# Kernel optimization log

Measured on AMD Instinct MI355X. Metric: run time of the kernel, lower is better.

The kernel has to match this reference:

```python
import jax, jax.numpy as jnp
import numpy as np

S, B, I, H = 2048, 64, 256, 128  # seq, batch, sent_size, hidden


def setup_inputs() -> dict:
    key = jax.random.key(0)
    ks = jax.random.split(key, 12)
    s = 1.0 / np.sqrt(H)
    u = lambda k, shape: jax.random.uniform(k, shape, jnp.float32, -s, s)
    return {
        "inp": jax.random.normal(ks[0], (S, B, I), jnp.float32),
        "hid_state": jax.random.normal(ks[1], (2, B, H), jnp.float32),
        "w_ih_f": u(ks[2], (3 * H, I)), "w_hh_f": u(ks[3], (3 * H, H)),
        "b_ih_f": u(ks[4], (3 * H,)), "b_hh_f": u(ks[5], (3 * H,)),
        "w_ih_b": u(ks[6], (3 * H, I)), "w_hh_b": u(ks[7], (3 * H, H)),
        "b_ih_b": u(ks[8], (3 * H,)), "b_hh_b": u(ks[9], (3 * H,)),
        "attn_w": u(ks[10], (2 * H, 2 * H)), "attn_b": jnp.zeros((2 * H,), jnp.float32),
        "comb_w": u(ks[11], (2 * H, 2 * H)),
    }


def _gru_dir(x, h0, w_ih, w_hh, b_ih, b_hh):
    # x: (S,B,I); precompute input-side gates once: (S,B,3H)
    xg = jnp.einsum('sbi,gi->sbg', x, w_ih) + b_ih

    def step(h, xg_t):
        gh = h @ w_hh.T + b_hh
        xr, xz, xn = jnp.split(xg_t, 3, axis=-1)
        hr, hz, hn = jnp.split(gh, 3, axis=-1)
        r = jax.nn.sigmoid(xr + hr)
        z = jax.nn.sigmoid(xz + hz)
        n = jnp.tanh(xn + r * hn)
        h_new = (1.0 - z) * n + z * h
        return h_new, h_new

    hT, outs = jax.lax.scan(step, h0, xg)
    return outs, hT


def reference(inp, hid_state, w_ih_f, w_hh_f, b_ih_f, b_hh_f,
              w_ih_b, w_hh_b, b_ih_b, b_hh_b, attn_w, attn_b, comb_w):
    out_f, hT_f = _gru_dir(inp, hid_state[0], w_ih_f, w_hh_f, b_ih_f, b_hh_f)
    out_b_rev, hT_b = _gru_dir(inp[::-1], hid_state[1], w_ih_b, w_hh_b, b_ih_b, b_hh_b)
    out_state = jnp.concatenate([out_f, out_b_rev[::-1]], axis=-1)  # (S,B,2H)
    hid_out = jnp.stack([hT_f, hT_b], axis=0)  # (2,B,H)
    sent_annotation = out_state @ attn_w.T + attn_b
    # NB: original applies softmax over dim=1 (the batch axis) — kept faithfully.
    attn = jax.nn.softmax(sent_annotation @ comb_w.T, axis=1)
    # fused multiply-reduce over seq (replaces the O(n) cat loop)
    sent = jnp.sum(attn * out_state, axis=0, keepdims=True)  # (1,B,2H)
    return sent, hid_out
```

## Files before the change

kernel.cpp:

```cpp
#include <hip/hip_runtime.h>
#include <cstdint>
#include <cstddef>

#define S_LEN 2048
#define BATCH 64
#define ISZ   256
#define HSZ   128

typedef __attribute__((ext_vector_type(8))) short short8;
typedef __attribute__((ext_vector_type(4))) float f32x4;

__device__ __forceinline__ uint32_t bfh(float x)
{
    uint32_t u = __float_as_uint(x);
    u += 0x7fffu + ((u >> 16) & 1u);
    return u >> 16;
}
__device__ __forceinline__ unsigned short f2bf(float x) { return (unsigned short)bfh(x); }

__device__ __forceinline__ void stage_tile(const float* __restrict__ src, int row0,
                                           int K, int k0, int tid,
                                           short* __restrict__ hi, short* __restrict__ lo)
{
    #pragma unroll
    for (int it = 0; it < 4; ++it) {
        const int g   = tid + it * 256;
        const int row = g >> 3;
        const int kg  = (g & 7) * 8;
        const float* p = src + (size_t)(row0 + row) * K + k0 + kg;
        const float4 v0 = *reinterpret_cast<const float4*>(p);
        const float4 v1 = *reinterpret_cast<const float4*>(p + 4);
        const float f[8] = {v0.x, v0.y, v0.z, v0.w, v1.x, v1.y, v1.z, v1.w};
        uint32_t hp[4], lp[4];
        #pragma unroll
        for (int i = 0; i < 4; ++i) {
            const uint32_t h0 = bfh(f[2*i]), h1 = bfh(f[2*i+1]);
            const float r0 = f[2*i]   - __uint_as_float(h0 << 16);
            const float r1 = f[2*i+1] - __uint_as_float(h1 << 16);
            hp[i] = h0 | (h1 << 16);
            lp[i] = bfh(r0) | (bfh(r1) << 16);
        }
        *reinterpret_cast<uint4*>(&hi[row*72 + kg]) = make_uint4(hp[0], hp[1], hp[2], hp[3]);
        *reinterpret_cast<uint4*>(&lo[row*72 + kg]) = make_uint4(lp[0], lp[1], lp[2], lp[3]);
    }
}

template<int LAYOUT>
__global__ __launch_bounds__(256, 2)
void gemm_mfma(const float* __restrict__ A, const float* __restrict__ W,
               const float* __restrict__ bias, float* __restrict__ C,
               int M, int N, int K)
{
    __shared__ short As_hi[128*72];
    __shared__ short As_lo[128*72];
    __shared__ short Ws_hi[128*72];
    __shared__ short Ws_lo[128*72];

    const int tid = threadIdx.x;
    const int wv  = tid >> 6;
    const int l   = tid & 63;
    const int fr  = l & 15;
    const int fk  = (l >> 4) * 8;
    const int m0  = blockIdx.y * 128;
    const int n0  = blockIdx.x * 128;

    f32x4 acc[2][8] = {};

    for (int k0 = 0; k0 < K; k0 += 64) {
        stage_tile(A, m0, K, k0, tid, As_hi, As_lo);
        stage_tile(W, n0, K, k0, tid, Ws_hi, Ws_lo);
        __syncthreads();

        #pragma unroll
        for (int ks = 0; ks < 64; ks += 32) {
            short8 ah[2], al[2], bh[8], bl[8];
            #pragma unroll
            for (int mt = 0; mt < 2; ++mt) {
                const int r = (wv*32 + mt*16 + fr) * 72 + ks + fk;
                ah[mt] = *reinterpret_cast<const short8*>(&As_hi[r]);
                al[mt] = *reinterpret_cast<const short8*>(&As_lo[r]);
            }
            #pragma unroll
            for (int nt = 0; nt < 8; ++nt) {
                const int r = (nt*16 + fr) * 72 + ks + fk;
                bh[nt] = *reinterpret_cast<const short8*>(&Ws_hi[r]);
                bl[nt] = *reinterpret_cast<const short8*>(&Ws_lo[r]);
            }
            #pragma unroll
            for (int mt = 0; mt < 2; ++mt) {
                #pragma unroll
                for (int nt = 0; nt < 8; ++nt) {
                    acc[mt][nt] = __builtin_amdgcn_mfma_f32_16x16x32_bf16(
                        ah[mt], bh[nt], acc[mt][nt], 0, 0, 0);
                    acc[mt][nt] = __builtin_amdgcn_mfma_f32_16x16x32_bf16(
                        ah[mt], bl[nt], acc[mt][nt], 0, 0, 0);
                    acc[mt][nt] = __builtin_amdgcn_mfma_f32_16x16x32_bf16(
                        al[mt], bh[nt], acc[mt][nt], 0, 0, 0);
                }
            }
        }
        __syncthreads();
    }

    const int orow = (l >> 4) * 4;
    #pragma unroll
    for (int nt = 0; nt < 8; ++nt) {
        const int n = n0 + nt*16 + fr;
        const float bv = bias ? bias[n] : 0.f;
        #pragma unroll
        for (int mt = 0; mt < 2; ++mt) {
            const int mbase = m0 + wv*32 + mt*16 + orow;
            const f32x4 a = acc[mt][nt];
            if (LAYOUT == 0) {
                #pragma unroll
                for (int r = 0; r < 4; ++r)
                    C[(size_t)(mbase + r) * N + n] = a[r] + bv;
            } else {
                float4 o;
                o.x = a[0] + bv; o.y = a[1] + bv; o.z = a[2] + bv; o.w = a[3] + bv;
                *reinterpret_cast<float4*>(
                    &C[(size_t)(mbase >> 6) * ((size_t)N * 64) +
                       (size_t)n * 64 + (mbase & 63)]) = o;
            }
        }
    }
}

#define GRU_NB 4

__global__ __launch_bounds__(512, 2)
void gru_mfma(const float* __restrict__ xg_f, const float* __restrict__ xg_b,
              const float* __restrict__ whh_f, const float* __restrict__ whh_b,
              const float* __restrict__ bhh_f, const float* __restrict__ bhh_b,
              const float* __restrict__ h0,
              float* __restrict__ outs,
              float* __restrict__ hid_out)
{
    const int tid = threadIdx.x;
    const int wv  = tid >> 6;
    const int l   = tid & 63;
    const int dir = blockIdx.x >> 4;
    const int bb  = blockIdx.x & 15;
    const int b0  = bb * GRU_NB;

    const float* xg  = dir ? xg_b  : xg_f;
    const float* whh = dir ? whh_b : whh_f;
    const float* bhh = dir ? bhh_b : bhh_f;

    __shared__ short hhi[16 * 136];
    __shared__ short hlo[16 * 136];
    __shared__ float gate[16 * 388];

    short8 afr[3][4];
    {
        const int arow = wv * 48 + (l & 15);
        const int akof = (l >> 4) * 8;
        #pragma unroll
        for (int rt = 0; rt < 3; ++rt) {
            #pragma unroll
            for (int ks = 0; ks < 4; ++ks) {
                const float* p = whh + (size_t)(arow + rt*16) * 128 + ks*32 + akof;
                const float4 v0 = *reinterpret_cast<const float4*>(p);
                const float4 v1 = *reinterpret_cast<const float4*>(p + 4);
                short8 s;
                s[0] = f2bf(v0.x); s[1] = f2bf(v0.y); s[2] = f2bf(v0.z); s[3] = f2bf(v0.w);
                s[4] = f2bf(v1.x); s[5] = f2bf(v1.y); s[6] = f2bf(v1.z); s[7] = f2bf(v1.w);
                afr[rt][ks] = s;
            }
        }
    }

    const int aj = tid & 127;
    const int ab = tid >> 7;
    const float bh_r = bhh[aj];
    const float bh_z = bhh[128 + aj];
    const float bh_n = bhh[256 + aj];

    for (int i = tid; i < 16 * 136; i += 512) { hhi[i] = 0; hlo[i] = 0; }
    __syncthreads();

    float hj = h0[dir * (64*128) + (b0 + ab) * 128 + aj];
    {
        const uint32_t hb = bfh(hj);
        hhi[ab * 136 + aj] = (short)hb;
        hlo[ab * 136 + aj] = (short)f2bf(hj - __uint_as_float(hb << 16));
    }
    float xr, xz, xn;
    {
        const int s0 = dir ? (S_LEN - 1) : 0;
        const float* xrow = xg + ((size_t)s0 * 64 + b0 + ab) * 384;
        xr = xrow[aj]; xz = xrow[aj + 128]; xn = xrow[aj + 256];
    }
    __syncthreads();

    const int brow = (l & 15) * 136;
    const int bkof = (l >> 4) * 8;
    const int gcol = (l & 15) * 388;
    const int grow0 = wv * 48 + (l >> 4) * 4;

    for (int t = 0; t < S_LEN; ++t) {
        float pxr = 0.f, pxz = 0.f, pxn = 0.f;
        if (t + 1 < S_LEN) {
            const int s1 = dir ? (S_LEN - 2 - t) : (t + 1);
            const float* xrow = xg + ((size_t)s1 * 64 + b0 + ab) * 384;
            pxr = xrow[aj]; pxz = xrow[aj + 128]; pxn = xrow[aj + 256];
        }

        f32x4 acc[3] = {};
        #pragma unroll
        for (int ks = 0; ks < 4; ++ks) {
            const short8 bh8 = *reinterpret_cast<const short8*>(&hhi[brow + ks*32 + bkof]);
            const short8 bl8 = *reinterpret_cast<const short8*>(&hlo[brow + ks*32 + bkof]);
            #pragma unroll
            for (int rt = 0; rt < 3; ++rt) {
                acc[rt] = __builtin_amdgcn_mfma_f32_16x16x32_bf16(afr[rt][ks], bh8, acc[rt], 0, 0, 0);
                acc[rt] = __builtin_amdgcn_mfma_f32_16x16x32_bf16(afr[rt][ks], bl8, acc[rt], 0, 0, 0);
            }
        }
        #pragma unroll
        for (int rt = 0; rt < 3; ++rt) {
            float4 o;
            o.x = acc[rt][0]; o.y = acc[rt][1]; o.z = acc[rt][2]; o.w = acc[rt][3];
            *reinterpret_cast<float4*>(&gate[gcol + grow0 + rt*16]) = o;
        }

        asm volatile("s_waitcnt lgkmcnt(0)" ::: "memory");
        __builtin_amdgcn_s_barrier();

        const float hr = gate[ab*388 + aj]       + bh_r;
        const float hz = gate[ab*388 + 128 + aj] + bh_z;
        const float hn = gate[ab*388 + 256 + aj] + bh_n;
        const float r = 1.f / (1.f + __expf(-(xr + hr)));
        const float z = 1.f / (1.f + __expf(-(xz + hz)));
        const float x2 = xn + r * hn;
        const float ax = fabsf(x2);
        const float e  = __expf(-2.f * ax);
        const float nn = copysignf((1.f - e) / (1.f + e), x2);
        const float hnew = nn + z * (hj - nn);
        hj = hnew;

        const int s = dir ? (S_LEN - 1 - t) : t;
        outs[((size_t)s * 64 + b0 + ab) * 256 + dir * 128 + aj] = hnew;

        const uint32_t hb = bfh(hnew);
        hhi[ab * 136 + aj] = (short)hb;
        hlo[ab * 136 + aj] = (short)f2bf(hnew - __uint_as_float(hb << 16));
        xr = pxr; xz = pxz; xn = pxn;

        asm volatile("s_waitcnt lgkmcnt(0)" ::: "memory");
        __builtin_amdgcn_s_barrier();
    }

    hid_out[dir * (64*128) + (b0 + ab) * 128 + aj] = hj;
}

__global__ __launch_bounds__(256)
void attn_reduce(const float* __restrict__ lt,
                 const float* __restrict__ outs,
                 float* __restrict__ part)
{
    __shared__ float ltile[64 * 64];
    __shared__ float otile[64 * 65];

    const int tid  = threadIdx.x;
    const int lane = tid & 63;
    const int wv   = tid >> 6;
    const int c0   = blockIdx.x * 64;
    const int sc   = blockIdx.y;

    float acc[16];
    #pragma unroll
    for (int i = 0; i < 16; ++i) acc[i] = 0.f;

    for (int si = 0; si < 32; ++si) {
        const int s = sc * 32 + si;

        const float4* src = reinterpret_cast<const float4*>(
            lt + (size_t)s * 16384 + (size_t)c0 * 64);
        #pragma unroll
        for (int i = 0; i < 4; ++i)
            reinterpret_cast<float4*>(ltile)[tid + i * 256] = src[tid + i * 256];

        #pragma unroll
        for (int i = 0; i < 4; ++i) {
            int idx = tid + i * 256;
            int bb = idx >> 4, c4 = (idx & 15) * 4;
            float4 v = *reinterpret_cast<const float4*>(
                &outs[((size_t)s * 64 + bb) * 256 + c0 + c4]);
            otile[bb*65 + c4+0] = v.x; otile[bb*65 + c4+1] = v.y;
            otile[bb*65 + c4+2] = v.z; otile[bb*65 + c4+3] = v.w;
        }
        __syncthreads();

        #pragma unroll
        for (int ci = 0; ci < 16; ++ci) {
            int c = wv * 16 + ci;
            float x = ltile[c * 64 + lane];
            float m = x;
            #pragma unroll
            for (int off = 32; off; off >>= 1)
                m = fmaxf(m, __shfl_xor(m, off));
            float e = __expf(x - m);
            float ssum = e;
            #pragma unroll
            for (int off = 32; off; off >>= 1)
                ssum += __shfl_xor(ssum, off);
            float attn = e / ssum;
            acc[ci] += attn * otile[lane * 65 + c];
        }
        __syncthreads();
    }

    #pragma unroll
    for (int ci = 0; ci < 16; ++ci) {
        int c = wv * 16 + ci;
        part[(size_t)sc * 16384 + (size_t)lane * 256 + c0 + c] = acc[ci];
    }
}

__global__ __launch_bounds__(256)
void reduce_part(const float* __restrict__ part, float* __restrict__ sent)
{
    int idx = blockIdx.x * 256 + threadIdx.x;
    float s = 0.f;
    for (int sc = 0; sc < 64; ++sc)
        s += part[(size_t)sc * 16384 + idx];
    sent[idx] = s;
}

extern "C" void kernel_launch(void* const* d_in, const int* in_sizes, int n_in,
                              void* d_out, int out_size, void* d_ws, size_t ws_size,
                              hipStream_t stream)
{
    const float* inp    = (const float*)d_in[0];
    const float* hid0   = (const float*)d_in[1];
    const float* w_ih_f = (const float*)d_in[2];
    const float* w_hh_f = (const float*)d_in[3];
    const float* b_ih_f = (const float*)d_in[4];
    const float* b_hh_f = (const float*)d_in[5];
    const float* w_ih_b = (const float*)d_in[6];
    const float* w_hh_b = (const float*)d_in[7];
    const float* b_ih_b = (const float*)d_in[8];
    const float* b_hh_b = (const float*)d_in[9];
    const float* attn_w = (const float*)d_in[10];
    const float* attn_b = (const float*)d_in[11];
    const float* comb_w = (const float*)d_in[12];

    float* out = (float*)d_out;

    char* ws = (char*)d_ws;
    const size_t XG_BYTES = (size_t)S_LEN * BATCH * 384 * 4;
    const size_t OS_BYTES = (size_t)S_LEN * BATCH * 256 * 4;
    if (ws_size < 2 * XG_BYTES + OS_BYTES) return;

    float* xg_f   = (float*)(ws);
    float* xg_b   = (float*)(ws + XG_BYTES);
    float* outs   = (float*)(ws + 2 * XG_BYTES);
    float* sa     = (float*)(ws);
    float* logits = (float*)(ws + XG_BYTES);
    float* part   = (float*)(ws);

    const int M = S_LEN * BATCH;
    dim3 blk(256);

    gemm_mfma<0><<<dim3(3, 1024), blk, 0, stream>>>(inp, w_ih_f, b_ih_f, xg_f, M, 384, 256);
    gemm_mfma<0><<<dim3(3, 1024), blk, 0, stream>>>(inp, w_ih_b, b_ih_b, xg_b, M, 384, 256);

    gru_mfma<<<dim3(32), dim3(512), 0, stream>>>(
        xg_f, xg_b, w_hh_f, w_hh_b, b_hh_f, b_hh_b, hid0, outs, out + 16384);

    gemm_mfma<0><<<dim3(2, 1024), blk, 0, stream>>>(outs, attn_w, attn_b, sa, M, 256, 256);

    gemm_mfma<1><<<dim3(2, 1024), blk, 0, stream>>>(sa, comb_w, nullptr, logits, M, 256, 256);

    attn_reduce<<<dim3(4, 64), blk, 0, stream>>>(logits, outs, part);

    reduce_part<<<dim3(64), blk, 0, stream>>>(part, out);
}
```

Baseline: 2.796 ms.

## Remap GRU gate rows per wave and double-buffer hidden state to drop a barrier

```diff
diff --git a/kernel.cpp b/kernel.cpp
--- a/kernel.cpp
+++ b/kernel.cpp
@@ -127,6 +127,22 @@
 }
 
 #define GRU_NB 4
+#define HPAD   144
+
+__device__ __forceinline__ void store_h4(short* __restrict__ hi, short* __restrict__ lo,
+                                         int off, float4 h)
+{
+    const uint32_t b0 = bfh(h.x), b1 = bfh(h.y), b2 = bfh(h.z), b3 = bfh(h.w);
+    ushort4 hv, lv;
+    hv.x = (unsigned short)b0; hv.y = (unsigned short)b1;
+    hv.z = (unsigned short)b2; hv.w = (unsigned short)b3;
+    lv.x = f2bf(h.x - __uint_as_float(b0 << 16));
+    lv.y = f2bf(h.y - __uint_as_float(b1 << 16));
+    lv.z = f2bf(h.z - __uint_as_float(b2 << 16));
+    lv.w = f2bf(h.w - __uint_as_float(b3 << 16));
+    *reinterpret_cast<ushort4*>(&hi[off]) = hv;
+    *reinterpret_cast<ushort4*>(&lo[off]) = lv;
+}
 
 __global__ __launch_bounds__(512, 2)
 void gru_mfma(const float* __restrict__ xg_f, const float* __restrict__ xg_b,
@@ -140,118 +156,126 @@
     const int wv  = tid >> 6;
     const int l   = tid & 63;
     const int dir = blockIdx.x >> 4;
-    const int bb  = blockIdx.x & 15;
-    const int b0  = bb * GRU_NB;
+    const int b0  = (blockIdx.x & 15) * GRU_NB;
 
     const float* xg  = dir ? xg_b  : xg_f;
     const float* whh = dir ? whh_b : whh_f;
     const float* bhh = dir ? bhh_b : bhh_f;
 
-    __shared__ short hhi[16 * 136];
-    __shared__ short hlo[16 * 136];
-    __shared__ float gate[16 * 388];
+    __shared__ short hhi[2 * 16 * HPAD];
+    __shared__ short hlo[2 * 16 * HPAD];
 
     short8 afr[3][4];
     {
-        const int arow = wv * 48 + (l & 15);
+        const int arow = wv * 16 + (l & 15);
         const int akof = (l >> 4) * 8;
         #pragma unroll
-        for (int rt = 0; rt < 3; ++rt) {
+        for (int g = 0; g < 3; ++g) {
             #pragma unroll
             for (int ks = 0; ks < 4; ++ks) {
-                const float* p = whh + (size_t)(arow + rt*16) * 128 + ks*32 + akof;
+                const float* p = whh + (size_t)(g*128 + arow) * 128 + ks*32 + akof;
                 const float4 v0 = *reinterpret_cast<const float4*>(p);
                 const float4 v1 = *reinterpret_cast<const float4*>(p + 4);
                 short8 s;
                 s[0] = f2bf(v0.x); s[1] = f2bf(v0.y); s[2] = f2bf(v0.z); s[3] = f2bf(v0.w);
                 s[4] = f2bf(v1.x); s[5] = f2bf(v1.y); s[6] = f2bf(v1.z); s[7] = f2bf(v1.w);
-                afr[rt][ks] = s;
-            }
-        }
-    }
-
-    const int aj = tid & 127;
-    const int ab = tid >> 7;
-    const float bh_r = bhh[aj];
-    const float bh_z = bhh[128 + aj];
-    const float bh_n = bhh[256 + aj];
-
-    for (int i = tid; i < 16 * 136; i += 512) { hhi[i] = 0; hlo[i] = 0; }
+                afr[g][ks] = s;
+            }
+        }
+    }
+
+    const int  bloc = l & 15;
+    const bool act  = bloc < GRU_NB;
+    const int  j0   = wv * 16 + (l >> 4) * 4;
+    const int  b    = b0 + bloc;
+
+    float4 br4 = {0,0,0,0}, bz4 = {0,0,0,0}, bn4 = {0,0,0,0};
+    float4 hj4 = {0,0,0,0};
+    if (act) {
+        br4 = *reinterpret_cast<const float4*>(&bhh[j0]);
+        bz4 = *reinterpret_cast<const float4*>(&bhh[128 + j0]);
+        bn4 = *reinterpret_cast<const float4*>(&bhh[256 + j0]);
+        hj4 = *reinterpret_cast<const float4*>(&h0[dir * (64*128) + b * 128 + j0]);
+    }
+
+    for (int i = tid; i < 2 * 16 * HPAD; i += 512) { hhi[i] = 0; hlo[i] = 0; }
     __syncthreads();
-
-    float hj = h0[dir * (64*128) + (b0 + ab) * 128 + aj];
-    {
-        const uint32_t hb = bfh(hj);
-        hhi[ab * 136 + aj] = (short)hb;
-        hlo[ab * 136 + aj] = (short)f2bf(hj - __uint_as_float(hb << 16));
-    }
-    float xr, xz, xn;
-    {
+    if (act) store_h4(hhi, hlo, bloc * HPAD + j0, hj4);
+
+    float4 xcr = {0,0,0,0}, xcz = {0,0,0,0}, xcn = {0,0,0,0};
+    float4 xnr = {0,0,0,0}, xnz = {0,0,0,0}, xnn = {0,0,0,0};
+    if (act) {
         const int s0 = dir ? (S_LEN - 1) : 0;
-        const float* xrow = xg + ((size_t)s0 * 64 + b0 + ab) * 384;
-        xr = xrow[aj]; xz = xrow[aj + 128]; xn = xrow[aj + 256];
+        const float* row = xg + ((size_t)s0 * 64 + b) * 384;
+        xcr = *reinterpret_cast<const float4*>(&row[j0]);
+        xcz = *reinterpret_cast<const float4*>(&row[128 + j0]);
+        xcn = *reinterpret_cast<const float4*>(&row[256 + j0]);
+        const int s1 = dir ? (S_LEN - 2) : 1;
+        const float* row1 = xg + ((size_t)s1 * 64 + b) * 384;
+        xnr = *reinterpret_cast<const float4*>(&row1[j0]);
+        xnz = *reinterpret_cast<const float4*>(&row1[128 + j0]);
+        xnn = *reinterpret_cast<const float4*>(&row1[256 + j0]);
     }
     __syncthreads();
 
-    const int brow = (l & 15) * 136;
+    const int brow = bloc * HPAD;
     const int bkof = (l >> 4) * 8;
-    const int gcol = (l & 15) * 388;
-    const int grow0 = wv * 48 + (l >> 4) * 4;
 
     for (int t = 0; t < S_LEN; ++t) {
-        float pxr = 0.f, pxz = 0.f, pxn = 0.f;
-        if (t + 1 < S_LEN) {
-            const int s1 = dir ? (S_LEN - 2 - t) : (t + 1);
-            const float* xrow = xg + ((size_t)s1 * 64 + b0 + ab) * 384;
-            pxr = xrow[aj]; pxz = xrow[aj + 128]; pxn = xrow[aj + 256];
-        }
-
-        f32x4 acc[3] = {};
+        const short* rhi = hhi + (t & 1) * (16 * HPAD);
+        const short* rlo = hlo + (t & 1) * (16 * HPAD);
+        short* whi = hhi + ((t + 1) & 1) * (16 * HPAD);
+        short* wlo = hlo + ((t + 1) & 1) * (16 * HPAD);
+
+        float4 xfr = {0,0,0,0}, xfz = {0,0,0,0}, xfn = {0,0,0,0};
+        if (act && t + 2 < S_LEN) {
+            const int s2 = dir ? (S_LEN - 3 - t) : (t + 2);
+            const float* row = xg + ((size_t)s2 * 64 + b) * 384;
+            xfr = *reinterpret_cast<const float4*>(&row[j0]);
+            xfz = *reinterpret_cast<const float4*>(&row[128 + j0]);
+            xfn = *reinterpret_cast<const float4*>(&row[256 + j0]);
+        }
+
+        f32x4 ach[3] = {}, acl[3] = {};
         #pragma unroll
         for (int ks = 0; ks < 4; ++ks) {
-            const short8 bh8 = *reinterpret_cast<const short8*>(&hhi[brow + ks*32 + bkof]);
-            const short8 bl8 = *reinterpret_cast<const short8*>(&hlo[brow + ks*32 + bkof]);
-            #pragma unroll
-            for (int rt = 0; rt < 3; ++rt) {
-                acc[rt] = __builtin_amdgcn_mfma_f32_16x16x32_bf16(afr[rt][ks], bh8, acc[rt], 0, 0, 0);
-                acc[rt] = __builtin_amdgcn_mfma_f32_16x16x32_bf16(afr[rt][ks], bl8, acc[rt], 0, 0, 0);
-            }
-        }
-        #pragma unroll
-        for (int rt = 0; rt < 3; ++rt) {
-            float4 o;
-            o.x = acc[rt][0]; o.y = acc[rt][1]; o.z = acc[rt][2]; o.w = acc[rt][3];
-            *reinterpret_cast<float4*>(&gate[gcol + grow0 + rt*16]) = o;
+            const short8 bh8 = *reinterpret_cast<const short8*>(&rhi[brow + ks*32 + bkof]);
+            const short8 bl8 = *reinterpret_cast<const short8*>(&rlo[brow + ks*32 + bkof]);
+            #pragma unroll
+            for (int g = 0; g < 3; ++g) {
+                ach[g] = __builtin_amdgcn_mfma_f32_16x16x32_bf16(afr[g][ks], bh8, ach[g], 0, 0, 0);
+                acl[g] = __builtin_amdgcn_mfma_f32_16x16x32_bf16(afr[g][ks], bl8, acl[g], 0, 0, 0);
+            }
+        }
+
+        if (act) {
+#define ACT1(I, C) { \
+            const float hr  = ach[0][I] + acl[0][I] + br4.C; \
+            const float hz  = ach[1][I] + acl[1][I] + bz4.C; \
+            const float hn_ = ach[2][I] + acl[2][I] + bn4.C; \
+            const float rr  = 1.f / (1.f + __expf(-(xcr.C + hr))); \
+            const float zz  = 1.f / (1.f + __expf(-(xcz.C + hz))); \
+            const float x2  = xcn.C + rr * hn_; \
+            const float ax  = fabsf(x2); \
+            const float ee  = __expf(-2.f * ax); \
+            const float nn  = copysignf((1.f - ee) / (1.f + ee), x2); \
+            hj4.C = nn + zz * (hj4.C - nn); }
+            ACT1(0, x) ACT1(1, y) ACT1(2, z) ACT1(3, w)
+#undef ACT1
+            const int s = dir ? (S_LEN - 1 - t) : t;
+            *reinterpret_cast<float4*>(
+                &outs[((size_t)s * 64 + b) * 256 + dir * 128 + j0]) = hj4;
+            store_h4(whi, wlo, brow + j0, hj4);
+            xcr = xnr; xcz = xnz; xcn = xnn;
+            xnr = xfr; xnz = xfz; xnn = xfn;
         }
 
         asm volatile("s_waitcnt lgkmcnt(0)" ::: "memory");
         __builtin_amdgcn_s_barrier();
-
-        const float hr = gate[ab*388 + aj]       + bh_r;
-        const float hz = gate[ab*388 + 128 + aj] + bh_z;
-        const float hn = gate[ab*388 + 256 + aj] + bh_n;
-        const float r = 1.f / (1.f + __expf(-(xr + hr)));
-        const float z = 1.f / (1.f + __expf(-(xz + hz)));
-        const float x2 = xn + r * hn;
-        const float ax = fabsf(x2);
-        const float e  = __expf(-2.f * ax);
-        const float nn = copysignf((1.f - e) / (1.f + e), x2);
-        const float hnew = nn + z * (hj - nn);
-        hj = hnew;
-
-        const int s = dir ? (S_LEN - 1 - t) : t;
-        outs[((size_t)s * 64 + b0 + ab) * 256 + dir * 128 + aj] = hnew;
-
-        const uint32_t hb = bfh(hnew);
-        hhi[ab * 136 + aj] = (short)hb;
-        hlo[ab * 136 + aj] = (short)f2bf(hnew - __uint_as_float(hb << 16));
-        xr = pxr; xz = pxz; xn = pxn;
-
-        asm volatile("s_waitcnt lgkmcnt(0)" ::: "memory");
-        __builtin_amdgcn_s_barrier();
-    }
-
-    hid_out[dir * (64*128) + (b0 + ab) * 128 + aj] = hj;
+    }
+
+    if (act)
+        *reinterpret_cast<float4*>(&hid_out[dir * (64*128) + b * 128 + j0]) = hj4;
 }
 
 __global__ __launch_bounds__(256)
```

Result: slower. 3.818 ms (+36.6%).
